# Kernel optimization log

Measured on AMD Instinct MI355X. Metric: run time of the kernel, lower is better.

Reference implementation:

```python
import jax, jax.numpy as jnp
import numpy as np

D_MODEL = 1024
N_HEAD = 16
D_K = D_MODEL // N_HEAD
D_FF = 2048
N_EXPERTS = 8
TOP_K = 2
B = 4
S = 1024
LN_EPS = 1e-5


def _layer_norm(x, g, b):
    mu = jnp.mean(x, axis=-1, keepdims=True)
    var = jnp.mean(jnp.square(x - mu), axis=-1, keepdims=True)
    return (x - mu) * jax.lax.rsqrt(var + LN_EPS) * g + b


def setup_inputs() -> dict:
    key = jax.random.key(0)
    ks = jax.random.split(key, 16)
    std = 0.02
    inp = {
        "x": jax.random.normal(ks[0], (B, S, D_MODEL), dtype=jnp.float32),
        "mask": jnp.ones((B, S, S), dtype=jnp.int32),
        "ln1_g": jnp.ones((D_MODEL,), jnp.float32),
        "ln1_b": jnp.zeros((D_MODEL,), jnp.float32),
        "wq": jax.random.normal(ks[1], (D_MODEL, D_MODEL), jnp.float32) * std,
        "wk": jax.random.normal(ks[2], (D_MODEL, D_MODEL), jnp.float32) * std,
        "wv": jax.random.normal(ks[3], (D_MODEL, D_MODEL), jnp.float32) * std,
        "wo": jax.random.normal(ks[4], (D_MODEL, D_MODEL), jnp.float32) * std,
        "wqd": jax.random.normal(ks[5], (D_MODEL, D_MODEL), jnp.float32) * std,
        "wkd": jax.random.normal(ks[6], (D_MODEL, D_MODEL), jnp.float32) * std,
        "wvd": jax.random.normal(ks[7], (D_MODEL, D_MODEL), jnp.float32) * std,
        "wod": jax.random.normal(ks[8], (D_MODEL, D_MODEL), jnp.float32) * std,
        "w_gate": jax.random.normal(ks[9], (D_MODEL, 2), jnp.float32) * std,
        "ln2_g": jnp.ones((D_MODEL,), jnp.float32),
        "ln2_b": jnp.zeros((D_MODEL,), jnp.float32),
        "w_router": jax.random.normal(ks[10], (D_MODEL, N_EXPERTS), jnp.float32) * std,
        "e_w1": jax.random.normal(ks[11], (N_EXPERTS, D_MODEL, D_FF), jnp.float32) * std,
        "e_w2": jax.random.normal(ks[12], (N_EXPERTS, D_FF, D_MODEL), jnp.float32) * std,
    }
    return inp


def _attention(x, mask, wq, wk, wv, wo, wqd, wkd, wvd, wod, w_gate):
    b, s, d = x.shape

    def split_heads(t):  # [b,s,d] -> [b,h,s,dk]
        return t.reshape(b, s, N_HEAD, D_K).transpose(0, 2, 1, 3)

    def merge_heads(t):  # [b,h,s,dk] -> [b,s,d]
        return t.transpose(0, 2, 1, 3).reshape(b, s, d)

    # dense attention branch
    q = split_heads(x @ wq)
    k = split_heads(x @ wk)
    v = split_heads(x @ wv)
    scores = jnp.einsum("bhqd,bhkd->bhqk", q, k) / jnp.sqrt(jnp.float32(D_K))
    scores = jnp.where(mask[:, None, :, :] == 0, jnp.float32(-1e9), scores)
    probs = jax.nn.softmax(scores, axis=-1)
    dense = merge_heads(jnp.einsum("bhqk,bhkd->bhqd", probs, v)) @ wo

    # linear delta attention branch (O(n))
    qd = split_heads(x @ wqd)
    kd = split_heads(x @ wkd)
    vd = split_heads(x @ wvd)
    q_lin = jax.nn.relu(qd)
    k_lin = jax.nn.relu(kd)
    # NOTE: original uses the *non-relu* k for the context matrix
    context = jnp.einsum("bhsd,bhse->bhde", kd, vd)  # [b,h,dk,dk]
    out = jnp.einsum("bhsd,bhde->bhse", q_lin, context)
    z = jnp.sum(q_lin * jnp.sum(k_lin, axis=-2, keepdims=True), axis=-1, keepdims=True) + 1e-6
    delta = merge_heads(out / z) @ wod

    gate = jax.nn.softmax(x @ w_gate, axis=-1)  # [b,s,2]
    return gate[..., 0:1] * dense + gate[..., 1:2] * delta


def _moe(x, w_router, e_w1, e_w2):
    b, s, d = x.shape
    xt = x.reshape(b * s, d)  # tokens
    logits = xt @ w_router  # [N, E]
    topk_logits, topk_idx = jax.lax.top_k(logits, TOP_K)
    topk_w = jax.nn.softmax(topk_logits, axis=-1)  # [N, K]
    # dense combine weights [N, E] (equivalent to masked gather/scatter-add)
    n = xt.shape[0]
    comb = jnp.zeros((n, N_EXPERTS), xt.dtype).at[jnp.arange(n)[:, None], topk_idx].add(topk_w)
    # all tokens through all experts (jit-friendly dense dispatch)
    h = jax.nn.gelu(jnp.einsum("nd,edf->enf", xt, e_w1), approximate=False)
    y = jnp.einsum("enf,efd->end", h, e_w2)
    out = jnp.einsum("end,ne->nd", y, comb)
    return out.reshape(b, s, d)


def reference(x, mask, ln1_g, ln1_b, wq, wk, wv, wo, wqd, wkd, wvd, wod, w_gate,
              ln2_g, ln2_b, w_router, e_w1, e_w2):
    x = x + _attention(_layer_norm(x, ln1_g, ln1_b), mask,
                       wq, wk, wv, wo, wqd, wkd, wvd, wod, w_gate)
    x = x + _moe(_layer_norm(x, ln2_g, ln2_b), w_router, e_w1, e_w2)
    return x
```

## Files before the change

### kernel.cpp

```cpp
#include <hip/hip_runtime.h>
#include <stdint.h>


typedef __attribute__((ext_vector_type(8))) short short8;
typedef __attribute__((ext_vector_type(4))) float floatx4;

#define DMODEL 1024
#define SEQ    1024
#define NHEAD  16
#define DK     64
#define DFF    2048
#define NEXP   8
#define MAXTILE 144

__device__ __forceinline__ float bf2f(unsigned short h){
  union{unsigned u;float f;}v; v.u=((unsigned)h)<<16; return v.f;
}
__device__ __forceinline__ unsigned short f2bf(float f){
  union{float f;unsigned u;}v; v.f=f;
  unsigned r=(v.u + 0x7FFFu + ((v.u>>16)&1u))>>16; return (unsigned short)r;
}
__device__ __forceinline__ void splitbf(float v, unsigned short& hi, unsigned short& lo){
  hi = f2bf(v); lo = f2bf(v - bf2f(hi));
}

__device__ __forceinline__ void glds16(const unsigned short* g, unsigned short* l){
  __builtin_amdgcn_global_load_lds(
      (const __attribute__((address_space(1))) void*)g,
      (__attribute__((address_space(3))) void*)l, 16, 0, 0);
}

__device__ __forceinline__ float block_sum(float v, float* red){
  for(int off=32;off;off>>=1) v += __shfl_down(v,off,64);
  int w = threadIdx.x>>6;
  __syncthreads();
  if((threadIdx.x&63)==0) red[w]=v;
  __syncthreads();
  return red[0]+red[1]+red[2]+red[3];
}

__global__ __launch_bounds__(256) void k_maskpack(
    const int* __restrict__ mask, unsigned long long* __restrict__ mp){
  int gw = blockIdx.x*4 + (threadIdx.x>>6);
  int lane = threadIdx.x&63;
  unsigned long long bm = __ballot(mask[(long)gw*64 + lane] != 0);
  if(lane==0) mp[gw]=bm;
}

__global__ __launch_bounds__(256) void k_transpose_f2(
    const float* __restrict__ src, unsigned short* __restrict__ dh,
    unsigned short* __restrict__ dl, long srs, long drs, long sbs, long dbs){
  __shared__ float t[32][33];
  src += (long)blockIdx.z*sbs; dh += (long)blockIdx.z*dbs; dl += (long)blockIdx.z*dbs;
  int c0 = blockIdx.x*32, r0 = blockIdx.y*32;
  int tx = threadIdx.x & 31, ty = threadIdx.x >> 5;
  for(int i=0;i<32;i+=8)
    t[ty+i][tx] = src[(long)(r0+ty+i)*srs + (c0+tx)];
  __syncthreads();
  for(int i=0;i<32;i+=8){
    unsigned short hi,lo; splitbf(t[tx][ty+i],hi,lo);
    long idx = (long)(c0+ty+i)*drs + (r0+tx);
    dh[idx]=hi; dl[idx]=lo;
  }
}

__global__ __launch_bounds__(256) void k_transpose_f(
    const float* __restrict__ src, unsigned short* __restrict__ dst,
    long srs, long drs, long sbs, long dbs){
  __shared__ float t[32][33];
  src += (long)blockIdx.z*sbs; dst += (long)blockIdx.z*dbs;
  int c0 = blockIdx.x*32, r0 = blockIdx.y*32;
  int tx = threadIdx.x & 31, ty = threadIdx.x >> 5;
  for(int i=0;i<32;i+=8)
    t[ty+i][tx] = src[(long)(r0+ty+i)*srs + (c0+tx)];
  __syncthreads();
  for(int i=0;i<32;i+=8)
    dst[(long)(c0+ty+i)*drs + (r0+tx)] = f2bf(t[tx][ty+i]);
}

__global__ __launch_bounds__(256) void k_vt3(
    const unsigned short* __restrict__ qh, const unsigned short* __restrict__ ql,
    unsigned short* __restrict__ vTh, unsigned short* __restrict__ vTl,
    unsigned short* __restrict__ kdTh, unsigned short* __restrict__ kdTl,
    unsigned short* __restrict__ vdTh, unsigned short* __restrict__ vdTl){
  __shared__ unsigned short th[32][33], tl[32][33];
  int z = blockIdx.z, b = z>>4, h = z&15;
  int slice = blockIdx.y >> 1;
  long coff = (slice==0) ? 2048 : (slice==1 ? 4096 : 5120);
  unsigned short* dh = (slice==0) ? vTh : (slice==1 ? kdTh : vdTh);
  unsigned short* dl = (slice==0) ? vTl : (slice==1 ? kdTl : vdTl);
  int s0 = blockIdx.x*32, d0 = (blockIdx.y&1)*32;
  int tx = threadIdx.x & 31, ty = threadIdx.x >> 5;
  for(int i=0;i<32;i+=8){
    long src = (long)(b*SEQ + s0+ty+i)*6144 + coff + h*DK + d0+tx;
    th[ty+i][tx] = qh[src]; tl[ty+i][tx] = ql[src];
  }
  __syncthreads();
  for(int i=0;i<32;i+=8){
    long dst = ((long)z*DK + d0+ty+i)*SEQ + s0+tx;
    dh[dst] = th[tx][ty+i]; dl[dst] = tl[tx][ty+i];
  }
}

__global__ __launch_bounds__(256) void k_ln1(
    const float* __restrict__ x, const float* __restrict__ g,
    const float* __restrict__ b, unsigned short* __restrict__ oh,
    unsigned short* __restrict__ ol){
  __shared__ float red[4];
  int t = blockIdx.x, tid = threadIdx.x;
  long base = (long)t*DMODEL + tid*4;
  floatx4 xv = *(const floatx4*)(x + base);
  float v[4] = {xv[0], xv[1], xv[2], xv[3]};
  float s = block_sum(v[0]+v[1]+v[2]+v[3], red);
  float mu = s * (1.f/DMODEL);
  float q=0.f;
  for(int i=0;i<4;i++){ float d=v[i]-mu; q+=d*d; }
  q = block_sum(q, red);
  float inv = rsqrtf(q*(1.f/DMODEL) + 1e-5f);
  for(int i=0;i<4;i++){
    int d = tid*4+i;
    unsigned short hi,lo; splitbf((v[i]-mu)*inv*g[d] + b[d], hi, lo);
    oh[base+i]=hi; ol[base+i]=lo;
  }
}

template<int SPLIT>
__global__ __launch_bounds__(256) void k_gemm128_ss(
    const unsigned short* __restrict__ Ah, const unsigned short* __restrict__ Al,
    const unsigned short* __restrict__ Bh, const unsigned short* __restrict__ Bl,
    unsigned short* __restrict__ Ch, unsigned short* __restrict__ Cl,
    float* __restrict__ Cf, int K, int lda, int ldb, int ldc, int gridN){
  __shared__ unsigned short Ash[128*32], Asl[128*32];
  __shared__ unsigned short Bsh[128*32], Bsl[128*32];
  int nwg = gridDim.x, bid = blockIdx.x;
  int swz = (bid & 7)*(nwg >> 3) + (bid >> 3);
  int bx = swz % gridN, by = swz / gridN;
  int m0 = by*128, n0 = bx*128;
  int tid = threadIdx.x, w = tid>>6, lane = tid&63;
  int qm = lane&15, quad = lane>>4;
  int wr = w>>1, wc = w&1;
  int lg = lane>>3, pp = lane&7, px = pp ^ lg;
  int rowl = (w<<4) + (lg<<1) + (px>>2);
  int c4s = (px&3)*8;
  int sdst = w*512 + lane*8;
  const unsigned short* pA0h = Ah + (long)(m0+rowl   )*lda + c4s;
  const unsigned short* pA1h = Ah + (long)(m0+rowl+64)*lda + c4s;
  const unsigned short* pA0l = Al + (long)(m0+rowl   )*lda + c4s;
  const unsigned short* pA1l = Al + (long)(m0+rowl+64)*lda + c4s;
  const unsigned short* pB0h = Bh + (long)(n0+rowl   )*ldb + c4s;
  const unsigned short* pB1h = Bh + (long)(n0+rowl+64)*ldb + c4s;
  const unsigned short* pB0l = Bl + (long)(n0+rowl   )*ldb + c4s;
  const unsigned short* pB1l = Bl + (long)(n0+rowl+64)*ldb + c4s;
  int fc = (((((qm&1)<<2)|quad) ^ (qm>>1))<<3);

  floatx4 acc[4][4];
  #pragma unroll
  for(int m=0;m<4;m++)
    #pragma unroll
    for(int n=0;n<4;n++) acc[m][n] = (floatx4){0.f,0.f,0.f,0.f};

  for(int k0=0;k0<K;k0+=32){
    __syncthreads();
    glds16(pA0h+k0, Ash+sdst); glds16(pA1h+k0, Ash+sdst+2048);
    glds16(pA0l+k0, Asl+sdst); glds16(pA1l+k0, Asl+sdst+2048);
    glds16(pB0h+k0, Bsh+sdst); glds16(pB1h+k0, Bsh+sdst+2048);
    glds16(pB0l+k0, Bsl+sdst); glds16(pB1l+k0, Bsl+sdst+2048);
    __syncthreads();
    short8 ah[4], al[4], bh[4], bl[4];
    #pragma unroll
    for(int m=0;m<4;m++){
      int ar = (wr*32 + m*8 + (qm>>1))*64 + fc;
      ah[m] = *(const short8*)(Ash+ar);
      al[m] = *(const short8*)(Asl+ar);
    }
    #pragma unroll
    for(int n=0;n<4;n++){
      int br = (wc*32 + n*8 + (qm>>1))*64 + fc;
      bh[n] = *(const short8*)(Bsh+br);
      bl[n] = *(const short8*)(Bsl+br);
    }
    #pragma unroll
    for(int m=0;m<4;m++)
      #pragma unroll
      for(int n=0;n<4;n++){
        acc[m][n] = __builtin_amdgcn_mfma_f32_16x16x32_bf16(ah[m],bh[n],acc[m][n],0,0,0);
        acc[m][n] = __builtin_amdgcn_mfma_f32_16x16x32_bf16(ah[m],bl[n],acc[m][n],0,0,0);
        acc[m][n] = __builtin_amdgcn_mfma_f32_16x16x32_bf16(al[m],bh[n],acc[m][n],0,0,0);
      }
  }
  #pragma unroll
  for(int m=0;m<4;m++){
    int row = m0 + wr*64 + m*16 + quad*4;
    #pragma unroll
    for(int r=0;r<4;r++){
      long rb = (long)(row+r)*ldc + n0 + wc*64;
      #pragma unroll
      for(int n=0;n<4;n++){
        float v = acc[m][n][r];
        if(SPLIT){
          unsigned short hi,lo; splitbf(v,hi,lo);
          Ch[rb+n*16+qm]=hi; Cl[rb+n*16+qm]=lo;
        }else{
          Cf[rb+n*16+qm]=v;
        }
      }
    }
  }
}

__global__ __launch_bounds__(256) void k_proj2(
    const unsigned short* __restrict__ dmh, const unsigned short* __restrict__ dml,
    const unsigned short* __restrict__ dlh, const unsigned short* __restrict__ dll,
    const unsigned short* __restrict__ WoTh, const unsigned short* __restrict__ WoTl,
    const unsigned short* __restrict__ WodTh, const unsigned short* __restrict__ WodTl,
    float* __restrict__ dproj, float* __restrict__ dlproj){
  __shared__ unsigned short Ash[128*32], Asl[128*32];
  __shared__ unsigned short Bsh[128*32], Bsl[128*32];
  int bid = blockIdx.x;
  int swz = (bid & 7)*64 + (bid >> 3);
  int which = swz >> 8, rem = swz & 255;
  int bx = rem & 7, by = rem >> 3;
  int m0 = by*128, n0 = bx*128;
  const unsigned short* Ah = which ? dlh : dmh;
  const unsigned short* Al = which ? dll : dml;
  const unsigned short* Bh = which ? WodTh : WoTh;
  const unsigned short* Bl = which ? WodTl : WoTl;
  float* Cf = which ? dlproj : dproj;
  int tid = threadIdx.x, w = tid>>6, lane = tid&63;
  int qm = lane&15, quad = lane>>4;
  int wr = w>>1, wc = w&1;
  int lg = lane>>3, pp = lane&7, px = pp ^ lg;
  int rowl = (w<<4) + (lg<<1) + (px>>2);
  int c4s = (px&3)*8;
  int sdst = w*512 + lane*8;
  const unsigned short* pA0h = Ah + (long)(m0+rowl   )*1024 + c4s;
  const unsigned short* pA1h = Ah + (long)(m0+rowl+64)*1024 + c4s;
  const unsigned short* pA0l = Al + (long)(m0+rowl   )*1024 + c4s;
  const unsigned short* pA1l = Al + (long)(m0+rowl+64)*1024 + c4s;
  const unsigned short* pB0h = Bh + (long)(n0+rowl   )*1024 + c4s;
  const unsigned short* pB1h = Bh + (long)(n0+rowl+64)*1024 + c4s;
  const unsigned short* pB0l = Bl + (long)(n0+rowl   )*1024 + c4s;
  const unsigned short* pB1l = Bl + (long)(n0+rowl+64)*1024 + c4s;
  int fc = (((((qm&1)<<2)|quad) ^ (qm>>1))<<3);

  floatx4 acc[4][4];
  #pragma unroll
  for(int m=0;m<4;m++)
    #pragma unroll
    for(int n=0;n<4;n++) acc[m][n] = (floatx4){0.f,0.f,0.f,0.f};

  for(int k0=0;k0<1024;k0+=32){
    __syncthreads();
    glds16(pA0h+k0, Ash+sdst); glds16(pA1h+k0, Ash+sdst+2048);
    glds16(pA0l+k0, Asl+sdst); glds16(pA1l+k0, Asl+sdst+2048);
    glds16(pB0h+k0, Bsh+sdst); glds16(pB1h+k0, Bsh+sdst+2048);
    glds16(pB0l+k0, Bsl+sdst); glds16(pB1l+k0, Bsl+sdst+2048);
    __syncthreads();
    short8 ah[4], al[4], bh[4], bl[4];
    #pragma unroll
    for(int m=0;m<4;m++){
      int ar = (wr*32 + m*8 + (qm>>1))*64 + fc;
      ah[m] = *(const short8*)(Ash+ar);
      al[m] = *(const short8*)(Asl+ar);
    }
    #pragma unroll
    for(int n=0;n<4;n++){
      int br = (wc*32 + n*8 + (qm>>1))*64 + fc;
      bh[n] = *(const short8*)(Bsh+br);
      bl[n] = *(const short8*)(Bsl+br);
    }
    #pragma unroll
    for(int m=0;m<4;m++)
      #pragma unroll
      for(int n=0;n<4;n++){
        acc[m][n] = __builtin_amdgcn_mfma_f32_16x16x32_bf16(ah[m],bh[n],acc[m][n],0,0,0);
        acc[m][n] = __builtin_amdgcn_mfma_f32_16x16x32_bf16(ah[m],bl[n],acc[m][n],0,0,0);
        acc[m][n] = __builtin_amdgcn_mfma_f32_16x16x32_bf16(al[m],bh[n],acc[m][n],0,0,0);
      }
  }
  #pragma unroll
  for(int m=0;m<4;m++){
    int row = m0 + wr*64 + m*16 + quad*4;
    #pragma unroll
    for(int r=0;r<4;r++){
      long rb = (long)(row+r)*1024 + n0 + wc*64;
      #pragma unroll
      for(int n=0;n<4;n++)
        Cf[rb+n*16+qm] = acc[m][n][r];
    }
  }
}

__global__ __launch_bounds__(256) void k_gate(
    const unsigned short* __restrict__ hh, const unsigned short* __restrict__ hl,
    const float* __restrict__ wg, float* __restrict__ gates){
  int token = blockIdx.x*4 + (threadIdx.x>>6);
  int lane = threadIdx.x&63;
  long hb = (long)token*DMODEL + lane*16;
  const float* w = wg + lane*16*2;
  float s0=0.f, s1=0.f;
  for(int i=0;i<16;i++){
    float hv = bf2f(hh[hb+i]) + bf2f(hl[hb+i]);
    s0 += hv*w[2*i]; s1 += hv*w[2*i+1];
  }
  for(int off=32;off;off>>=1){ s0+=__shfl_down(s0,off,64); s1+=__shfl_down(s1,off,64); }
  if(lane==0){
    float m=fmaxf(s0,s1), e0=__expf(s0-m), e1=__expf(s1-m), inv=1.f/(e0+e1);
    gates[token*2]=e0*inv; gates[token*2+1]=e1*inv;
  }
}

__global__ __launch_bounds__(256) void k_attn_flash3(
    const unsigned short* __restrict__ qh, const unsigned short* __restrict__ qlp,
    const unsigned short* __restrict__ vth, const unsigned short* __restrict__ vtl,
    const unsigned long long* __restrict__ mp, unsigned short* __restrict__ dmh,
    unsigned short* __restrict__ dml){
  __shared__ unsigned short Ksh[64*64], Ksl[64*64];
  __shared__ unsigned short Vsh[64*64], Vsl[64*64];
  __shared__ unsigned short PWh[4*16*64], PWl[4*16*64];
  int bh = blockIdx.y, b = bh>>4, h = bh&15;
  int tid = threadIdx.x, w = tid>>6, lane = tid&63;
  int qm = lane&15, quad = (lane>>4)&3;
  int q0 = blockIdx.x*64 + w*16;
  long qrow = (long)(b*SEQ+q0+qm)*6144 + h*DK;
  short8 a_qh0 = *(const short8*)(qh +qrow+quad*8);
  short8 a_qh1 = *(const short8*)(qh +qrow+32+quad*8);
  short8 a_ql0 = *(const short8*)(qlp+qrow+quad*8);
  short8 a_ql1 = *(const short8*)(qlp+qrow+32+quad*8);
  float m[4], l[4];
  floatx4 o0={0,0,0,0}, o1={0,0,0,0}, o2={0,0,0,0}, o3={0,0,0,0};
  #pragma unroll
  for(int r=0;r<4;r++){ m[r]=-3.0e38f; l[r]=0.f; }
  const unsigned long long* mrow = mp + ((long)b*SEQ + q0 + quad*4)*16;

  int r8 = lane>>3;
  int c8 = (lane&7) ^ r8;
  int d0 = w*512 + lane*8;
  const unsigned short* pKh0 = qh  + (long)(b*SEQ + w*8 + r8)*6144 + 1024 + h*DK + c8*8;
  const unsigned short* pKl0 = qlp + (long)(b*SEQ + w*8 + r8)*6144 + 1024 + h*DK + c8*8;
  const unsigned short* pKh1 = pKh0 + 32L*6144;
  const unsigned short* pKl1 = pKl0 + 32L*6144;
  const unsigned short* pVh0 = vth + ((long)bh*DK + w*8 + r8)*SEQ + c8*8;
  const unsigned short* pVl0 = vtl + ((long)bh*DK + w*8 + r8)*SEQ + c8*8;
  const unsigned short* pVh1 = pVh0 + 32L*SEQ;
  const unsigned short* pVl1 = pVl0 + 32L*SEQ;
  int q7 = qm&7;

  for(int kt=0; kt<SEQ; kt+=64){
    __syncthreads();
    long ko = (long)kt*6144;
    glds16(pKh0+ko, Ksh+d0); glds16(pKh1+ko, Ksh+d0+2048);
    glds16(pKl0+ko, Ksl+d0); glds16(pKl1+ko, Ksl+d0+2048);
    glds16(pVh0+kt, Vsh+d0); glds16(pVh1+kt, Vsh+d0+2048);
    glds16(pVl0+kt, Vsl+d0); glds16(pVl1+kt, Vsl+d0+2048);
    __syncthreads();

    int wd = kt>>6;
    unsigned long long mws[4] = {mrow[wd], mrow[16+wd], mrow[32+wd], mrow[48+wd]};
    floatx4 s[4];
    #pragma unroll
    for(int st=0;st<4;st++){
      int krow = (st*16+qm)*64;
      short8 kh0 = *(const short8*)(Ksh + krow + ((quad    ^q7)<<3));
      short8 kh1 = *(const short8*)(Ksh + krow + (((4|quad)^q7)<<3));
      short8 kl0 = *(const short8*)(Ksl + krow + ((quad    ^q7)<<3));
      short8 kl1 = *(const short8*)(Ksl + krow + (((4|quad)^q7)<<3));
      floatx4 acc = {0,0,0,0};
      acc = __builtin_amdgcn_mfma_f32_16x16x32_bf16(a_qh0,kh0,acc,0,0,0);
      acc = __builtin_amdgcn_mfma_f32_16x16x32_bf16(a_qh1,kh1,acc,0,0,0);
      acc = __builtin_amdgcn_mfma_f32_16x16x32_bf16(a_qh0,kl0,acc,0,0,0);
      acc = __builtin_amdgcn_mfma_f32_16x16x32_bf16(a_qh1,kl1,acc,0,0,0);
      acc = __builtin_amdgcn_mfma_f32_16x16x32_bf16(a_ql0,kh0,acc,0,0,0);
      acc = __builtin_amdgcn_mfma_f32_16x16x32_bf16(a_ql1,kh1,acc,0,0,0);
      s[st] = acc;
    }
    #pragma unroll
    for(int r=0;r<4;r++){
      float v0 = ((mws[r]>>(   qm))&1) ? s[0][r]*0.125f : -1e9f;
      float v1 = ((mws[r]>>(16+qm))&1) ? s[1][r]*0.125f : -1e9f;
      float v2 = ((mws[r]>>(32+qm))&1) ? s[2][r]*0.125f : -1e9f;
      float v3 = ((mws[r]>>(48+qm))&1) ? s[3][r]*0.125f : -1e9f;
      float tm = fmaxf(fmaxf(v0,v1), fmaxf(v2,v3));
      tm = fmaxf(tm, __shfl_xor(tm,1,16));
      tm = fmaxf(tm, __shfl_xor(tm,2,16));
      tm = fmaxf(tm, __shfl_xor(tm,4,16));
      tm = fmaxf(tm, __shfl_xor(tm,8,16));
      float nm = fmaxf(m[r], tm);
      float al = __expf(m[r]-nm);
      m[r] = nm;
      float p0=__expf(v0-nm), p1=__expf(v1-nm), p2=__expf(v2-nm), p3=__expf(v3-nm);
      float rs = p0+p1+p2+p3;
      rs += __shfl_xor(rs,1,16); rs += __shfl_xor(rs,2,16);
      rs += __shfl_xor(rs,4,16); rs += __shfl_xor(rs,8,16);
      l[r] = l[r]*al + rs;
      o0[r]*=al; o1[r]*=al; o2[r]*=al; o3[r]*=al;
      int row = quad*4+r, rsw = row&7;
      int pb = w*1024 + row*64 + (qm&7);
      unsigned short hi,lo;
      splitbf(p0,hi,lo); PWh[pb + ((( (qm>>3))^rsw)<<3)]=hi; PWl[pb + ((( (qm>>3))^rsw)<<3)]=lo;
      splitbf(p1,hi,lo); PWh[pb + (((2|(qm>>3))^rsw)<<3)]=hi; PWl[pb + (((2|(qm>>3))^rsw)<<3)]=lo;
      splitbf(p2,hi,lo); PWh[pb + (((4|(qm>>3))^rsw)<<3)]=hi; PWl[pb + (((4|(qm>>3))^rsw)<<3)]=lo;
      splitbf(p3,hi,lo); PWh[pb + (((6|(qm>>3))^rsw)<<3)]=hi; PWl[pb + (((6|(qm>>3))^rsw)<<3)]=lo;
    }
    __builtin_amdgcn_wave_barrier();
    int prb = w*1024 + qm*64;
    short8 ph0 = *(const short8*)(PWh + prb + ((quad    ^q7)<<3));
    short8 ph1 = *(const short8*)(PWh + prb + (((4|quad)^q7)<<3));
    short8 pl0 = *(const short8*)(PWl + prb + ((quad    ^q7)<<3));
    short8 pl1 = *(const short8*)(PWl + prb + (((4|quad)^q7)<<3));
    __builtin_amdgcn_wave_barrier();
    {
      int c0 = (quad    ^q7)<<3;
      int c1 = ((4|quad)^q7)<<3;
      int vr0 = (0*16+qm)*64, vr1 = (1*16+qm)*64, vr2 = (2*16+qm)*64, vr3 = (3*16+qm)*64;
      short8 v0h0=*(const short8*)(Vsh+vr0+c0), v0h1=*(const short8*)(Vsh+vr0+c1);
      short8 v1h0=*(const short8*)(Vsh+vr1+c0), v1h1=*(const short8*)(Vsh+vr1+c1);
      short8 v2h0=*(const short8*)(Vsh+vr2+c0), v2h1=*(const short8*)(Vsh+vr2+c1);
      short8 v3h0=*(const short8*)(Vsh+vr3+c0), v3h1=*(const short8*)(Vsh+vr3+c1);
      short8 v0l0=*(const short8*)(Vsl+vr0+c0), v0l1=*(const short8*)(Vsl+vr0+c1);
      short8 v1l0=*(const short8*)(Vsl+vr1+c0), v1l1=*(const short8*)(Vsl+vr1+c1);
      short8 v2l0=*(const short8*)(Vsl+vr2+c0), v2l1=*(const short8*)(Vsl+vr2+c1);
      short8 v3l0=*(const short8*)(Vsl+vr3+c0), v3l1=*(const short8*)(Vsl+vr3+c1);
      o0 = __builtin_amdgcn_mfma_f32_16x16x32_bf16(ph0,v0h0,o0,0,0,0);
      o0 = __builtin_amdgcn_mfma_f32_16x16x32_bf16(ph1,v0h1,o0,0,0,0);
      o0 = __builtin_amdgcn_mfma_f32_16x16x32_bf16(ph0,v0l0,o0,0,0,0);
      o0 = __builtin_amdgcn_mfma_f32_16x16x32_bf16(ph1,v0l1,o0,0,0,0);
      o0 = __builtin_amdgcn_mfma_f32_16x16x32_bf16(pl0,v0h0,o0,0,0,0);
      o0 = __builtin_amdgcn_mfma_f32_16x16x32_bf16(pl1,v0h1,o0,0,0,0);
      o1 = __builtin_amdgcn_mfma_f32_16x16x32_bf16(ph0,v1h0,o1,0,0,0);
      o1 = __builtin_amdgcn_mfma_f32_16x16x32_bf16(ph1,v1h1,o1,0,0,0);
      o1 = __builtin_amdgcn_mfma_f32_16x16x32_bf16(ph0,v1l0,o1,0,0,0);
      o1 = __builtin_amdgcn_mfma_f32_16x16x32_bf16(ph1,v1l1,o1,0,0,0);
      o1 = __builtin_amdgcn_mfma_f32_16x16x32_bf16(pl0,v1h0,o1,0,0,0);
      o1 = __builtin_amdgcn_mfma_f32_16x16x32_bf16(pl1,v1h1,o1,0,0,0);
      o2 = __builtin_amdgcn_mfma_f32_16x16x32_bf16(ph0,v2h0,o2,0,0,0);
      o2 = __builtin_amdgcn_mfma_f32_16x16x32_bf16(ph1,v2h1,o2,0,0,0);
      o2 = __builtin_amdgcn_mfma_f32_16x16x32_bf16(ph0,v2l0,o2,0,0,0);
      o2 = __builtin_amdgcn_mfma_f32_16x16x32_bf16(ph1,v2l1,o2,0,0,0);
      o2 = __builtin_amdgcn_mfma_f32_16x16x32_bf16(pl0,v2h0,o2,0,0,0);
      o2 = __builtin_amdgcn_mfma_f32_16x16x32_bf16(pl1,v2h1,o2,0,0,0);
      o3 = __builtin_amdgcn_mfma_f32_16x16x32_bf16(ph0,v3h0,o3,0,0,0);
      o3 = __builtin_amdgcn_mfma_f32_16x16x32_bf16(ph1,v3h1,o3,0,0,0);
      o3 = __builtin_amdgcn_mfma_f32_16x16x32_bf16(ph0,v3l0,o3,0,0,0);
      o3 = __builtin_amdgcn_mfma_f32_16x16x32_bf16(ph1,v3l1,o3,0,0,0);
      o3 = __builtin_amdgcn_mfma_f32_16x16x32_bf16(pl0,v3h0,o3,0,0,0);
      o3 = __builtin_amdgcn_mfma_f32_16x16x32_bf16(pl1,v3h1,o3,0,0,0);
    }
  }
  #pragma unroll
  for(int r=0;r<4;r++){
    float inv = 1.f/l[r];
    long rb = ((long)(b*SEQ + q0 + quad*4 + r))*DMODEL + h*DK;
    unsigned short hi,lo;
    splitbf(o0[r]*inv,hi,lo); dmh[rb+   qm]=hi; dml[rb+   qm]=lo;
    splitbf(o1[r]*inv,hi,lo); dmh[rb+16+qm]=hi; dml[rb+16+qm]=lo;
    splitbf(o2[r]*inv,hi,lo); dmh[rb+32+qm]=hi; dml[rb+32+qm]=lo;
    splitbf(o3[r]*inv,hi,lo); dmh[rb+48+qm]=hi; dml[rb+48+qm]=lo;
  }
}

__global__ __launch_bounds__(256) void k_delta_ctx2(
    const unsigned short* __restrict__ kdTh, const unsigned short* __restrict__ kdTl,
    const unsigned short* __restrict__ vdTh, const unsigned short* __restrict__ vdTl,
    float* __restrict__ ctx, float* __restrict__ ksum){
  int bh = blockIdx.x;
  int tid = threadIdx.x, w = tid>>6, lane = tid&63;
  int qm = lane&15, quad = lane>>4;
  long abase = ((long)bh*DK + w*16 + qm)*SEQ + quad*8;
  long bbase = ((long)bh*DK + qm)*SEQ + quad*8;
  floatx4 acc[4];
  #pragma unroll
  for(int n=0;n<4;n++) acc[n] = (floatx4){0.f,0.f,0.f,0.f};
  float ks = 0.f;
  #pragma unroll 2
  for(int s0=0;s0<SEQ;s0+=32){
    short8 ah = *(const short8*)(kdTh + abase + s0);
    short8 al = *(const short8*)(kdTl + abase + s0);
    #pragma unroll
    for(int j=0;j<8;j++)
      ks += fmaxf(bf2f((unsigned short)ah[j]) + bf2f((unsigned short)al[j]), 0.f);
    #pragma unroll
    for(int n=0;n<4;n++){
      short8 bh8 = *(const short8*)(vdTh + bbase + (long)n*16*SEQ + s0);
      short8 bl8 = *(const short8*)(vdTl + bbase + (long)n*16*SEQ + s0);
      acc[n] = __builtin_amdgcn_mfma_f32_16x16x32_bf16(ah,bh8,acc[n],0,0,0);
      acc[n] = __builtin_amdgcn_mfma_f32_16x16x32_bf16(ah,bl8,acc[n],0,0,0);
      acc[n] = __builtin_amdgcn_mfma_f32_16x16x32_bf16(al,bh8,acc[n],0,0,0);
    }
  }
  long cb = (long)bh*DK*DK;
  #pragma unroll
  for(int n=0;n<4;n++)
    #pragma unroll
    for(int r=0;r<4;r++)
      ctx[cb + (long)(w*16 + quad*4 + r)*DK + n*16 + qm] = acc[n][r];
  ks += __shfl_xor(ks,16,64);
  ks += __shfl_xor(ks,32,64);
  if(quad==0) ksum[bh*DK + w*16 + qm] = ks;
}

__global__ __launch_bounds__(256) void k_delta_out(
    const unsigned short* __restrict__ qh, const unsigned short* __restrict__ qlp,
    const float* __restrict__ ctx, const float* __restrict__ ksum,
    unsigned short* __restrict__ dlh, unsigned short* __restrict__ dll){
  int tok = blockIdx.x, b = tok>>10;
  int tid = threadIdx.x;
  __shared__ float ql[DMODEL];
  long sb = (long)tok*6144 + 3072;
  for(int c=tid;c<DMODEL;c+=256)
    ql[c] = fmaxf(bf2f(qh[sb+c]) + bf2f(qlp[sb+c]), 0.f);
  __syncthreads();
  int h = tid>>4, dg = (tid&15)*4;
  int bh = b*NHEAD + h;
  const float* C = ctx + (long)bh*DK*DK;
  const float* KS = ksum + bh*DK;
  float a0=0,a1=0,a2=0,a3=0,z=0;
  for(int d=0;d<DK;d++){
    float q = ql[h*DK + d];
    z += q * KS[d];
    const float* cr = C + d*DK + dg;
    a0 += q*cr[0]; a1 += q*cr[1]; a2 += q*cr[2]; a3 += q*cr[3];
  }
  float inv = 1.f/(z + 1e-6f);
  long db = (long)tok*DMODEL + h*DK + dg;
  unsigned short hi,lo;
  splitbf(a0*inv,hi,lo); dlh[db  ]=hi; dll[db  ]=lo;
  splitbf(a1*inv,hi,lo); dlh[db+1]=hi; dll[db+1]=lo;
  splitbf(a2*inv,hi,lo); dlh[db+2]=hi; dll[db+2]=lo;
  splitbf(a3*inv,hi,lo); dlh[db+3]=hi; dll[db+3]=lo;
}

__global__ __launch_bounds__(256) void k_comb_router(
    const float* __restrict__ x, const float* __restrict__ dp,
    const float* __restrict__ dlp, const float* __restrict__ gates,
    const float* __restrict__ g, const float* __restrict__ bb,
    const float* __restrict__ wr, unsigned short* __restrict__ h2b,
    float* __restrict__ topw, int* __restrict__ topi, int* __restrict__ counts){
  __shared__ float red[4];
  __shared__ float ered[4][8];
  int t = blockIdx.x, tid = threadIdx.x;
  float g0 = gates[t*2], g1 = gates[t*2+1];
  long base = (long)t*DMODEL + tid*4;
  floatx4 xv = *(const floatx4*)(x + base);
  float v[4];
  for(int i=0;i<4;i++) v[i] = xv[i] + g0*dp[base+i] + g1*dlp[base+i];
  float s = block_sum(v[0]+v[1]+v[2]+v[3], red);
  float mu = s*(1.f/DMODEL);
  float q=0.f; for(int i=0;i<4;i++){ float d=v[i]-mu; q+=d*d; }
  q = block_sum(q, red);
  float inv = rsqrtf(q*(1.f/DMODEL)+1e-5f);
  float a[8]; for(int e=0;e<8;e++) a[e]=0.f;
  for(int i=0;i<4;i++){
    int d = tid*4+i;
    float hv = (v[i]-mu)*inv*g[d] + bb[d];
    h2b[base+i] = f2bf(hv);
    const float* wrow = wr + (long)d*NEXP;
    for(int e=0;e<8;e++) a[e] += hv*wrow[e];
  }
  for(int off=32;off;off>>=1)
    for(int e=0;e<8;e++) a[e] += __shfl_down(a[e],off,64);
  int w = tid>>6;
  if((tid&63)==0) for(int e=0;e<8;e++) ered[w][e]=a[e];
  __syncthreads();
  if(tid==0){
    float lg[8];
    for(int e=0;e<8;e++) lg[e]=ered[0][e]+ered[1][e]+ered[2][e]+ered[3][e];
    int i0=0; for(int e=1;e<8;e++) if(lg[e]>lg[i0]) i0=e;
    int i1=-1; for(int e=0;e<8;e++){ if(e==i0) continue; if(i1<0||lg[e]>lg[i1]) i1=e; }
    float mm=fmaxf(lg[i0],lg[i1]), e0=__expf(lg[i0]-mm), e1=__expf(lg[i1]-mm), s2=1.f/(e0+e1);
    topw[t*2]=e0*s2; topw[t*2+1]=e1*s2;
    topi[t*2]=i0; topi[t*2+1]=i1;
    atomicAdd(&counts[i0],1); atomicAdd(&counts[i1],1);
  }
}

__global__ void k_meta(const int* __restrict__ counts, int* offs, int* tE,
                       int* tR0, int* tR1, int* ntp, int* cursor){
  if(threadIdx.x==0){
    int o=0, nt=0;
    for(int e=0;e<NEXP;e++){
      offs[e]=o; cursor[e]=0;
      int n=counts[e];
      for(int t=0;t<(n+127)/128;t++){ tE[nt]=e; tR0[nt]=o+t*128; tR1[nt]=o+n; nt++; }
      o+=n;
    }
    offs[NEXP]=o; ntp[0]=nt;
  }
}

__global__ __launch_bounds__(256) void k_scatter(
    const int* __restrict__ topi, const int* __restrict__ offs,
    int* cursor, int* perm, int* slotof){
  int token = blockIdx.x*256 + threadIdx.x;
  for(int k=0;k<2;k++){
    int e = topi[token*2+k];
    int pos = atomicAdd(&cursor[e],1);
    int slot = offs[e]+pos;
    perm[slot]=token; slotof[token*2+k]=slot;
  }
}

template<int GELU, int GATHER>
__global__ __launch_bounds__(256) void k_moe128(
    const unsigned short* __restrict__ A, const unsigned short* __restrict__ BtA,
    unsigned short* __restrict__ C, const int* __restrict__ perm,
    const int* __restrict__ ntp, const int* __restrict__ tE,
    const int* __restrict__ tR0, const int* __restrict__ tR1,
    int K, int N){
  int bz = blockIdx.y;
  if(bz >= ntp[0]) return;
  int e = tE[bz], r0t = tR0[bz], r1t = tR1[bz];
  __shared__ unsigned short As[128*32], Bs[128*32];
  int tid = threadIdx.x, w = tid>>6, lane = tid&63;
  int qm = lane&15, quad = lane>>4;
  int wr = w>>1, wc = w&1;
  int n0 = blockIdx.x*128;
  int lg = lane>>3, pp = lane&7, px = pp ^ lg;
  int rowl = (w<<4) + (lg<<1) + (px>>2);
  int c4s = (px&3)*8;
  int sdst = w*512 + lane*8;
  int fc = (((((qm&1)<<2)|quad) ^ (qm>>1))<<3);
  int gr0 = r0t + rowl, gr1 = gr0 + 64;
  int gc0 = gr0 < 8191 ? gr0 : 8191;
  int gc1 = gr1 < 8191 ? gr1 : 8191;
  const unsigned short *pA0, *pA1;
  if(GATHER){
    pA0 = A + (long)perm[gc0]*K + c4s;
    pA1 = A + (long)perm[gc1]*K + c4s;
  }else{
    pA0 = A + (long)gc0*K + c4s;
    pA1 = A + (long)gc1*K + c4s;
  }
  const unsigned short* Bt = BtA + (long)e*N*K;
  const unsigned short* pB0 = Bt + (long)(n0+rowl   )*K + c4s;
  const unsigned short* pB1 = Bt + (long)(n0+rowl+64)*K + c4s;

  floatx4 acc[4][4];
  #pragma unroll
  for(int m=0;m<4;m++)
    #pragma unroll
    for(int n=0;n<4;n++) acc[m][n] = (floatx4){0.f,0.f,0.f,0.f};

  for(int k0=0;k0<K;k0+=32){
    __syncthreads();
    glds16(pA0+k0, As+sdst); glds16(pA1+k0, As+sdst+2048);
    glds16(pB0+k0, Bs+sdst); glds16(pB1+k0, Bs+sdst+2048);
    __syncthreads();
    short8 af[4], bf[4];
    #pragma unroll
    for(int m=0;m<4;m++)
      af[m] = *(const short8*)(As + (wr*32 + m*8 + (qm>>1))*64 + fc);
    #pragma unroll
    for(int n=0;n<4;n++)
      bf[n] = *(const short8*)(Bs + (wc*32 + n*8 + (qm>>1))*64 + fc);
    #pragma unroll
    for(int m=0;m<4;m++)
      #pragma unroll
      for(int n=0;n<4;n++)
        acc[m][n] = __builtin_amdgcn_mfma_f32_16x16x32_bf16(af[m],bf[n],acc[m][n],0,0,0);
  }
  #pragma unroll
  for(int m=0;m<4;m++){
    int row = r0t + wr*64 + m*16 + quad*4;
    #pragma unroll
    for(int r=0;r<4;r++){
      if(row+r < r1t){
        long rb = (long)(row+r)*N + n0 + wc*64;
        #pragma unroll
        for(int n=0;n<4;n++){
          float xx = acc[m][n][r];
          if(GELU) xx = 0.5f*xx*(1.f+erff(xx*0.70710678f));
          C[rb+n*16+qm] = f2bf(xx);
        }
      }
    }
  }
}

__global__ __launch_bounds__(256) void k_final(
    const float* __restrict__ x, const float* __restrict__ dp,
    const float* __restrict__ dlp, const float* __restrict__ gates,
    const unsigned short* __restrict__ Y, const int* __restrict__ slotof,
    const float* __restrict__ topw, float* __restrict__ out){
  int t = blockIdx.x, tid = threadIdx.x;
  int s0 = slotof[t*2], s1 = slotof[t*2+1];
  float w0 = topw[t*2], w1 = topw[t*2+1];
  float g0 = gates[t*2], g1 = gates[t*2+1];
  long base = (long)t*DMODEL + tid*4;
  const unsigned short* y0 = Y + (long)s0*DMODEL + tid*4;
  const unsigned short* y1 = Y + (long)s1*DMODEL + tid*4;
  floatx4 xv = *(const floatx4*)(x + base);
  for(int i=0;i<4;i++)
    out[base+i] = xv[i] + g0*dp[base+i] + g1*dlp[base+i]
                        + w0*bf2f(y0[i]) + w1*bf2f(y1[i]);
}

extern "C" void kernel_launch(void* const* d_in, const int* in_sizes, int n_in,
                              void* d_out, int out_size, void* d_ws, size_t ws_size,
                              hipStream_t stream){
  const float* x    = (const float*)d_in[0];
  const int*   mask = (const int*)d_in[1];
  const float* ln1g = (const float*)d_in[2];
  const float* ln1b = (const float*)d_in[3];
  const float* wq   = (const float*)d_in[4];
  const float* wk   = (const float*)d_in[5];
  const float* wv   = (const float*)d_in[6];
  const float* wo   = (const float*)d_in[7];
  const float* wqd  = (const float*)d_in[8];
  const float* wkd  = (const float*)d_in[9];
  const float* wvd  = (const float*)d_in[10];
  const float* wod  = (const float*)d_in[11];
  const float* wg   = (const float*)d_in[12];
  const float* ln2g = (const float*)d_in[13];
  const float* ln2b = (const float*)d_in[14];
  const float* wr   = (const float*)d_in[15];
  const float* ew1  = (const float*)d_in[16];
  const float* ew2  = (const float*)d_in[17];
  float* out = (float*)d_out;

  char* p = (char*)d_ws;
  auto alloc = [&](size_t b)->char*{ char* r=p; p += (b + 255) & ~(size_t)255; return r; };
  unsigned short* WtAllh = (unsigned short*)alloc(6144L*1024*2);
  unsigned short* WtAlll = (unsigned short*)alloc(6144L*1024*2);
  unsigned short* WoTh   = (unsigned short*)alloc(1024L*1024*2);
  unsigned short* WoTl   = (unsigned short*)alloc(1024L*1024*2);
  unsigned short* WodTh  = (unsigned short*)alloc(1024L*1024*2);
  unsigned short* WodTl  = (unsigned short*)alloc(1024L*1024*2);
  unsigned short* eW1T   = (unsigned short*)alloc(8L*2048*1024*2);
  unsigned short* eW2T   = (unsigned short*)alloc(8L*1024*2048*2);
  unsigned short* h1h    = (unsigned short*)alloc(4096L*1024*2);
  unsigned short* h1l    = (unsigned short*)alloc(4096L*1024*2);
  unsigned short* qkvh   = (unsigned short*)alloc(4096L*6144*2);
  unsigned short* qkvl   = (unsigned short*)alloc(4096L*6144*2);
  unsigned short* dmh    = (unsigned short*)alloc(4096L*1024*2);
  unsigned short* dml    = (unsigned short*)alloc(4096L*1024*2);
  unsigned short* dlh    = (unsigned short*)alloc(4096L*1024*2);
  unsigned short* dll    = (unsigned short*)alloc(4096L*1024*2);
  float* ctx   = (float*)alloc(64L*64*64*4);
  float* ksum  = (float*)alloc(64L*64*4);
  float* gates = (float*)alloc(4096L*2*4);
  unsigned short* h2b = (unsigned short*)alloc(4096L*1024*2);
  float* topw = (float*)alloc(4096L*2*4);
  int* topi   = (int*)alloc(4096L*2*4);
  int* slotof = (int*)alloc(4096L*2*4);
  int* perm   = (int*)alloc(8192L*4);
  int* counts = (int*)alloc(64*4);
  int* cursor = (int*)alloc(64*4);
  int* offs   = (int*)alloc(64*4);
  int* ntp    = (int*)alloc(64*4);
  int* tE     = (int*)alloc(MAXTILE*4);
  int* tR0    = (int*)alloc(MAXTILE*4);
  int* tR1    = (int*)alloc(MAXTILE*4);
  unsigned long long* mpack = (unsigned long long*)alloc(4L*1024*16*8);
  if ((size_t)(p - (char*)d_ws) > ws_size) return;

  unsigned short* vTh = h1h;
  unsigned short* vTl = h1l;
  unsigned short* kdTh = dlh;
  unsigned short* kdTl = dll;
  unsigned short* vdTh = dmh;
  unsigned short* vdTl = dml;
  float* dproj  = (float*)qkvh;
  float* dlproj = (float*)(qkvh + 8388608);
  unsigned short* H = qkvl;
  unsigned short* Y = dmh;

  dim3 tb(256);
  k_maskpack<<<16384,tb,0,stream>>>(mask, mpack);
  k_transpose_f2<<<dim3(32,32,1),tb,0,stream>>>(wq,  WtAllh+0L*1048576, WtAlll+0L*1048576, 1024,1024, 0,0);
  k_transpose_f2<<<dim3(32,32,1),tb,0,stream>>>(wk,  WtAllh+1L*1048576, WtAlll+1L*1048576, 1024,1024, 0,0);
  k_transpose_f2<<<dim3(32,32,1),tb,0,stream>>>(wv,  WtAllh+2L*1048576, WtAlll+2L*1048576, 1024,1024, 0,0);
  k_transpose_f2<<<dim3(32,32,1),tb,0,stream>>>(wqd, WtAllh+3L*1048576, WtAlll+3L*1048576, 1024,1024, 0,0);
  k_transpose_f2<<<dim3(32,32,1),tb,0,stream>>>(wkd, WtAllh+4L*1048576, WtAlll+4L*1048576, 1024,1024, 0,0);
  k_transpose_f2<<<dim3(32,32,1),tb,0,stream>>>(wvd, WtAllh+5L*1048576, WtAlll+5L*1048576, 1024,1024, 0,0);
  k_transpose_f2<<<dim3(32,32,1),tb,0,stream>>>(wo,  WoTh,  WoTl,  1024,1024, 0,0);
  k_transpose_f2<<<dim3(32,32,1),tb,0,stream>>>(wod, WodTh, WodTl, 1024,1024, 0,0);
  k_transpose_f<<<dim3(64,32,8),tb,0,stream>>>(ew1, eW1T, 2048,1024, 1024L*2048, 2048L*1024);
  k_transpose_f<<<dim3(32,64,8),tb,0,stream>>>(ew2, eW2T, 1024,2048, 2048L*1024, 1024L*2048);
  k_ln1<<<4096,tb,0,stream>>>(x, ln1g, ln1b, h1h, h1l);
  k_gemm128_ss<1><<<dim3(1536),tb,0,stream>>>(h1h,h1l, WtAllh,WtAlll, qkvh,qkvl,nullptr,
                                              1024, 1024, 1024, 6144, 48);
  k_gate<<<1024,tb,0,stream>>>(h1h, h1l, wg, gates);
  k_vt3<<<dim3(32,6,64),tb,0,stream>>>(qkvh, qkvl, vTh, vTl, kdTh, kdTl, vdTh, vdTl);
  k_delta_ctx2<<<64,tb,0,stream>>>(kdTh, kdTl, vdTh, vdTl, ctx, ksum);
  k_attn_flash3<<<dim3(16,64),tb,0,stream>>>(qkvh, qkvl, vTh, vTl, mpack, dmh, dml);
  k_delta_out<<<4096,tb,0,stream>>>(qkvh, qkvl, ctx, ksum, dlh, dll);
  k_proj2<<<dim3(512),tb,0,stream>>>(dmh,dml, dlh,dll, WoTh,WoTl, WodTh,WodTl,
                                     dproj, dlproj);
  hipMemsetAsync(counts, 0, NEXP*sizeof(int), stream);
  k_comb_router<<<4096,tb,0,stream>>>(x, dproj, dlproj, gates, ln2g, ln2b, wr,
                                      h2b, topw, topi, counts);
  k_meta<<<1,64,0,stream>>>(counts, offs, tE, tR0, tR1, ntp, cursor);
  k_scatter<<<16,tb,0,stream>>>(topi, offs, cursor, perm, slotof);
  k_moe128<1,1><<<dim3(16,72),tb,0,stream>>>(h2b, eW1T, H, perm, ntp, tE, tR0, tR1,
                                             1024, 2048);
  k_moe128<0,0><<<dim3(8,72),tb,0,stream>>>(H, eW2T, Y, perm, ntp, tE, tR0, tR1,
                                            2048, 1024);
  k_final<<<4096,tb,0,stream>>>(x, dproj, dlproj, gates, Y, slotof, topw, out);
}
```

Before: 1.003 ms.

## Double K-step per barrier in proj2 and MoE GEMMs, remap gemm128 block swizzle

```diff
diff --git a/kernel.cpp b/kernel.cpp
--- a/kernel.cpp
+++ b/kernel.cpp
@@ -133,8 +133,9 @@
   __shared__ unsigned short Ash[128*32], Asl[128*32];
   __shared__ unsigned short Bsh[128*32], Bsl[128*32];
   int nwg = gridDim.x, bid = blockIdx.x;
-  int swz = (bid & 7)*(nwg >> 3) + (bid >> 3);
-  int bx = swz % gridN, by = swz / gridN;
+  int g = bid & 7, r = bid >> 3;
+  int rpx = (nwg / gridN) >> 3;
+  int bx = r / rpx, by = g*rpx + (r % rpx);
   int m0 = by*128, n0 = bx*128;
   int tid = threadIdx.x, w = tid>>6, lane = tid&63;
   int qm = lane&15, quad = lane>>4;
@@ -192,11 +193,11 @@
   for(int m=0;m<4;m++){
     int row = m0 + wr*64 + m*16 + quad*4;
     #pragma unroll
-    for(int r=0;r<4;r++){
-      long rb = (long)(row+r)*ldc + n0 + wc*64;
+    for(int r2=0;r2<4;r2++){
+      long rb = (long)(row+r2)*ldc + n0 + wc*64;
       #pragma unroll
       for(int n=0;n<4;n++){
-        float v = acc[m][n][r];
+        float v = acc[m][n][r2];
         if(SPLIT){
           unsigned short hi,lo; splitbf(v,hi,lo);
           Ch[rb+n*16+qm]=hi; Cl[rb+n*16+qm]=lo;
@@ -214,8 +215,8 @@
     const unsigned short* __restrict__ WoTh, const unsigned short* __restrict__ WoTl,
     const unsigned short* __restrict__ WodTh, const unsigned short* __restrict__ WodTl,
     float* __restrict__ dproj, float* __restrict__ dlproj){
-  __shared__ unsigned short Ash[128*32], Asl[128*32];
-  __shared__ unsigned short Bsh[128*32], Bsl[128*32];
+  __shared__ unsigned short Ash[128*64], Asl[128*64];
+  __shared__ unsigned short Bsh[128*64], Bsl[128*64];
   int bid = blockIdx.x;
   int swz = (bid & 7)*64 + (bid >> 3);
   int which = swz >> 8, rem = swz & 255;
@@ -249,34 +250,42 @@
     #pragma unroll
     for(int n=0;n<4;n++) acc[m][n] = (floatx4){0.f,0.f,0.f,0.f};
 
-  for(int k0=0;k0<1024;k0+=32){
+  for(int k0=0;k0<1024;k0+=64){
     __syncthreads();
-    glds16(pA0h+k0, Ash+sdst); glds16(pA1h+k0, Ash+sdst+2048);
-    glds16(pA0l+k0, Asl+sdst); glds16(pA1l+k0, Asl+sdst+2048);
-    glds16(pB0h+k0, Bsh+sdst); glds16(pB1h+k0, Bsh+sdst+2048);
-    glds16(pB0l+k0, Bsl+sdst); glds16(pB1l+k0, Bsl+sdst+2048);
+    glds16(pA0h+k0,    Ash+sdst);      glds16(pA1h+k0,    Ash+sdst+2048);
+    glds16(pA0h+k0+32, Ash+4096+sdst); glds16(pA1h+k0+32, Ash+4096+sdst+2048);
+    glds16(pA0l+k0,    Asl+sdst);      glds16(pA1l+k0,    Asl+sdst+2048);
+    glds16(pA0l+k0+32, Asl+4096+sdst); glds16(pA1l+k0+32, Asl+4096+sdst+2048);
+    glds16(pB0h+k0,    Bsh+sdst);      glds16(pB1h+k0,    Bsh+sdst+2048);
+    glds16(pB0h+k0+32, Bsh+4096+sdst); glds16(pB1h+k0+32, Bsh+4096+sdst+2048);
+    glds16(pB0l+k0,    Bsl+sdst);      glds16(pB1l+k0,    Bsl+sdst+2048);
+    glds16(pB0l+k0+32, Bsl+4096+sdst); glds16(pB1l+k0+32, Bsl+4096+sdst+2048);
     __syncthreads();
-    short8 ah[4], al[4], bh[4], bl[4];
-    #pragma unroll
-    for(int m=0;m<4;m++){
-      int ar = (wr*32 + m*8 + (qm>>1))*64 + fc;
-      ah[m] = *(const short8*)(Ash+ar);
-      al[m] = *(const short8*)(Asl+ar);
-    }
-    #pragma unroll
-    for(int n=0;n<4;n++){
-      int br = (wc*32 + n*8 + (qm>>1))*64 + fc;
-      bh[n] = *(const short8*)(Bsh+br);
-      bl[n] = *(const short8*)(Bsl+br);
-    }
-    #pragma unroll
-    for(int m=0;m<4;m++)
+    #pragma unroll
+    for(int c=0;c<2;c++){
+      int cb = c*4096;
+      short8 ah[4], al[4], bh[4], bl[4];
+      #pragma unroll
+      for(int m=0;m<4;m++){
+        int ar = cb + (wr*32 + m*8 + (qm>>1))*64 + fc;
+        ah[m] = *(const short8*)(Ash+ar);
+        al[m] = *(const short8*)(Asl+ar);
+      }
       #pragma unroll
       for(int n=0;n<4;n++){
-        acc[m][n] = __builtin_amdgcn_mfma_f32_16x16x32_bf16(ah[m],bh[n],acc[m][n],0,0,0);
-        acc[m][n] = __builtin_amdgcn_mfma_f32_16x16x32_bf16(ah[m],bl[n],acc[m][n],0,0,0);
-        acc[m][n] = __builtin_amdgcn_mfma_f32_16x16x32_bf16(al[m],bh[n],acc[m][n],0,0,0);
+        int br = cb + (wc*32 + n*8 + (qm>>1))*64 + fc;
+        bh[n] = *(const short8*)(Bsh+br);
+        bl[n] = *(const short8*)(Bsl+br);
       }
+      #pragma unroll
+      for(int m=0;m<4;m++)
+        #pragma unroll
+        for(int n=0;n<4;n++){
+          acc[m][n] = __builtin_amdgcn_mfma_f32_16x16x32_bf16(ah[m],bh[n],acc[m][n],0,0,0);
+          acc[m][n] = __builtin_amdgcn_mfma_f32_16x16x32_bf16(ah[m],bl[n],acc[m][n],0,0,0);
+          acc[m][n] = __builtin_amdgcn_mfma_f32_16x16x32_bf16(al[m],bh[n],acc[m][n],0,0,0);
+        }
+    }
   }
   #pragma unroll
   for(int m=0;m<4;m++){
@@ -610,7 +619,7 @@
   int bz = blockIdx.y;
   if(bz >= ntp[0]) return;
   int e = tE[bz], r0t = tR0[bz], r1t = tR1[bz];
-  __shared__ unsigned short As[128*32], Bs[128*32];
+  __shared__ unsigned short As[128*64], Bs[128*64];
   int tid = threadIdx.x, w = tid>>6, lane = tid&63;
   int qm = lane&15, quad = lane>>4;
   int wr = w>>1, wc = w&1;
@@ -641,23 +650,29 @@
     #pragma unroll
     for(int n=0;n<4;n++) acc[m][n] = (floatx4){0.f,0.f,0.f,0.f};
 
-  for(int k0=0;k0<K;k0+=32){
+  for(int k0=0;k0<K;k0+=64){
     __syncthreads();
-    glds16(pA0+k0, As+sdst); glds16(pA1+k0, As+sdst+2048);
-    glds16(pB0+k0, Bs+sdst); glds16(pB1+k0, Bs+sdst+2048);
+    glds16(pA0+k0,    As+sdst);      glds16(pA1+k0,    As+sdst+2048);
+    glds16(pA0+k0+32, As+4096+sdst); glds16(pA1+k0+32, As+4096+sdst+2048);
+    glds16(pB0+k0,    Bs+sdst);      glds16(pB1+k0,    Bs+sdst+2048);
+    glds16(pB0+k0+32, Bs+4096+sdst); glds16(pB1+k0+32, Bs+4096+sdst+2048);
     __syncthreads();
-    short8 af[4], bf[4];
-    #pragma unroll
-    for(int m=0;m<4;m++)
-      af[m] = *(const short8*)(As + (wr*32 + m*8 + (qm>>1))*64 + fc);
-    #pragma unroll
-    for(int n=0;n<4;n++)
-      bf[n] = *(const short8*)(Bs + (wc*32 + n*8 + (qm>>1))*64 + fc);
-    #pragma unroll
-    for(int m=0;m<4;m++)
+    #pragma unroll
+    for(int c=0;c<2;c++){
+      int cb = c*4096;
+      short8 af[4], bf[4];
+      #pragma unroll
+      for(int m=0;m<4;m++)
+        af[m] = *(const short8*)(As + cb + (wr*32 + m*8 + (qm>>1))*64 + fc);
       #pragma unroll
       for(int n=0;n<4;n++)
-        acc[m][n] = __builtin_amdgcn_mfma_f32_16x16x32_bf16(af[m],bf[n],acc[m][n],0,0,0);
+        bf[n] = *(const short8*)(Bs + cb + (wc*32 + n*8 + (qm>>1))*64 + fc);
+      #pragma unroll
+      for(int m=0;m<4;m++)
+        #pragma unroll
+        for(int n=0;n<4;n++)
+          acc[m][n] = __builtin_amdgcn_mfma_f32_16x16x32_bf16(af[m],bf[n],acc[m][n],0,0,0);
+    }
   }
   #pragma unroll
   for(int m=0;m<4;m++){
```

Measured after the change: 971.4 us. -3.2%, faster.
